# Kernel tuning notes

Measured on AMD Instinct MI355X. Metric: run time of the kernel, lower is better.

Reference implementation:

```python
import jax, jax.numpy as jnp
import numpy as np

B, H, S, D = 4, 16, 2048, 128

def setup_inputs() -> dict:
    key = jax.random.key(0)
    kq, kk, kv = jax.random.split(key, 3)
    query = jax.random.normal(kq, (B, H, S, D), dtype=jnp.float32)
    k = jax.random.normal(kk, (B, H, S, D), dtype=jnp.float32)
    value = jax.random.normal(kv, (B, H, S, D), dtype=jnp.float32)
    attn_mask = jnp.zeros((B, H, S, S), dtype=jnp.float32)
    return {"query": query, "key": k, "value": value, "attn_mask": attn_mask}

def reference(query, key, value, attn_mask):
    # scores: [B,H,S,S]
    scale = 1.0 / jnp.sqrt(jnp.asarray(query.shape[-1], query.dtype))
    scores = jnp.einsum('bhqd,bhkd->bhqk', query, key) * scale + attn_mask
    attn = jax.nn.softmax(scores, axis=-1)
    out = jnp.einsum('bhqk,bhkd->bhqd', attn, value)
    return out
```

## Files before the change

### kernel.cpp

```cpp
#include <hip/hip_runtime.h>

#define SDIM 2048
#define DDIM 128
#define NBH  64
#define BR   128
#define BC   64
#define PSTRIDE 72

using bf16x8 = __attribute__((ext_vector_type(8))) short;
using f32x4  = __attribute__((ext_vector_type(4))) float;

static __device__ __forceinline__ short f2bf(float x) {
    unsigned u = __float_as_uint(x);
    u += 0x7fff + ((u >> 16) & 1);
    return (short)(u >> 16);
}
static __device__ __forceinline__ unsigned pack2(float a, float b) {
    return ((unsigned)(unsigned short)f2bf(a)) |
           (((unsigned)(unsigned short)f2bf(b)) << 16);
}

__global__ __launch_bounds__(256) void kconv_kernel(const float* __restrict__ K,
                                                    unsigned short* __restrict__ Kc)
{
    size_t i = ((size_t)blockIdx.x * 256 + threadIdx.x) * 4;
    float4 v = *(const float4*)(K + i);
    uint2 o;
    o.x = pack2(v.x, v.y);
    o.y = pack2(v.z, v.w);
    *(uint2*)(Kc + i) = o;
}

__global__ __launch_bounds__(256) void vtrans_kernel(const float* __restrict__ V,
                                                     unsigned short* __restrict__ Vt)
{
    __shared__ float t[32][33];
    const int bh = blockIdx.z;
    const int s0 = blockIdx.x * 32;
    const int d0 = blockIdx.y * 32;
    const int x = threadIdx.x & 31;
    const int y = threadIdx.x >> 5;
    const float* Vb = V + (size_t)bh * SDIM * DDIM;
    unsigned short* Vtb = Vt + (size_t)bh * SDIM * DDIM;
#pragma unroll
    for (int i = 0; i < 4; ++i) {
        int r = y + i * 8;
        t[r][x] = Vb[(size_t)(s0 + r) * DDIM + d0 + x];
    }
    __syncthreads();
#pragma unroll
    for (int i = 0; i < 4; ++i) {
        int r = y + i * 8;
        Vtb[(size_t)(d0 + r) * SDIM + s0 + x] = (unsigned short)f2bf(t[x][r]);
    }
}

static __device__ __forceinline__ void load_mask(const float* __restrict__ Mb,
                                                 int q0, int wave, int quad, int n16,
                                                 int kcol, float (&mk)[2][4][4])
{
#pragma unroll
    for (int rt = 0; rt < 2; ++rt) {
        const int rowb = q0 + wave * 32 + rt * 16 + quad * 4;
        const float* mpb = Mb + (size_t)rowb * SDIM + kcol + n16;
#pragma unroll
        for (int ct = 0; ct < 4; ++ct)
#pragma unroll
            for (int r = 0; r < 4; ++r)
                mk[rt][ct][r] = mpb[(size_t)r * SDIM + ct * 16];
    }
}

static __device__ __forceinline__ void ktile_body(
    int k0, int q0, int wave, int quad, int n16, int lane,
    const float* __restrict__ Mb,
    const unsigned short* __restrict__ Kb, const unsigned short* __restrict__ Vb,
    unsigned short* __restrict__ PsW,
    const bf16x8 (&qf)[2][4],
    f32x4 (&acc)[2][8], float (&mrow)[2][4], float (&lrow)[2][4],
    float (&mkc)[2][4][4], float (&mkn)[2][4][4])
{
    const f32x4 zero4 = {0.f, 0.f, 0.f, 0.f};

    f32x4 s[2][4];
#pragma unroll
    for (int rt = 0; rt < 2; ++rt)
#pragma unroll
        for (int ct = 0; ct < 4; ++ct) s[rt][ct] = zero4;
#pragma unroll
    for (int dt = 0; dt < 4; ++dt) {
#pragma unroll
        for (int ct = 0; ct < 4; ++ct) {
            bf16x8 kf = *(const bf16x8*)(Kb + (size_t)(k0 + ct * 16 + n16) * DDIM + dt * 32 + quad * 8);
            s[0][ct] = __builtin_amdgcn_mfma_f32_16x16x32_bf16(qf[0][dt], kf, s[0][ct], 0, 0, 0);
            s[1][ct] = __builtin_amdgcn_mfma_f32_16x16x32_bf16(qf[1][dt], kf, s[1][ct], 0, 0, 0);
        }
    }

    __builtin_amdgcn_sched_barrier(0);
    load_mask(Mb, q0, wave, quad, n16, (k0 + BC) & (SDIM - 1), mkn);
    __builtin_amdgcn_sched_barrier(0);

#pragma unroll
    for (int rt = 0; rt < 2; ++rt)
#pragma unroll
        for (int ct = 0; ct < 4; ++ct)
#pragma unroll
            for (int r = 0; r < 4; ++r)
                s[rt][ct][r] += mkc[rt][ct][r];

    float mx[2][4];
#pragma unroll
    for (int rt = 0; rt < 2; ++rt)
#pragma unroll
        for (int r = 0; r < 4; ++r)
            mx[rt][r] = fmaxf(fmaxf(s[rt][0][r], s[rt][1][r]),
                              fmaxf(s[rt][2][r], s[rt][3][r]));
#pragma unroll
    for (int st = 1; st <= 8; st <<= 1)
#pragma unroll
        for (int rt = 0; rt < 2; ++rt)
#pragma unroll
            for (int r = 0; r < 4; ++r)
                mx[rt][r] = fmaxf(mx[rt][r], __shfl_xor(mx[rt][r], st));

    int anynew = 0;
#pragma unroll
    for (int rt = 0; rt < 2; ++rt)
#pragma unroll
        for (int r = 0; r < 4; ++r)
            anynew |= (mx[rt][r] > mrow[rt][r]) ? 1 : 0;
    if (__ballot(anynew) != 0ull) {
#pragma unroll
        for (int rt = 0; rt < 2; ++rt)
#pragma unroll
            for (int r = 0; r < 4; ++r) {
                float mnew = fmaxf(mrow[rt][r], mx[rt][r]);
                float al = exp2f((mrow[rt][r] - mnew) * 1.44269504f);
                mrow[rt][r] = mnew;
                lrow[rt][r] *= al;
#pragma unroll
                for (int nt = 0; nt < 8; ++nt) acc[rt][nt][r] *= al;
            }
    }

    float rs[2][4];
#pragma unroll
    for (int rt = 0; rt < 2; ++rt)
#pragma unroll
        for (int r = 0; r < 4; ++r) {
            float t = 0.f;
#pragma unroll
            for (int ct = 0; ct < 4; ++ct) {
                float pv = exp2f((s[rt][ct][r] - mrow[rt][r]) * 1.44269504f);
                s[rt][ct][r] = pv;
                t += pv;
            }
            rs[rt][r] = t;
        }
#pragma unroll
    for (int st = 1; st <= 8; st <<= 1)
#pragma unroll
        for (int rt = 0; rt < 2; ++rt)
#pragma unroll
            for (int r = 0; r < 4; ++r)
                rs[rt][r] += __shfl_xor(rs[rt][r], st);
#pragma unroll
    for (int rt = 0; rt < 2; ++rt)
#pragma unroll
        for (int r = 0; r < 4; ++r)
            lrow[rt][r] += rs[rt][r];

#pragma unroll
    for (int rt = 0; rt < 2; ++rt)
#pragma unroll
        for (int ct = 0; ct < 4; ++ct)
#pragma unroll
            for (int r = 0; r < 4; ++r)
                PsW[(rt * 16 + (lane >> 4) * 4 + r) * PSTRIDE + ct * 16 + n16] =
                    (unsigned short)f2bf(s[rt][ct][r]);

    bf16x8 pa[2][2];
#pragma unroll
    for (int rt = 0; rt < 2; ++rt)
#pragma unroll
        for (int kt = 0; kt < 2; ++kt)
            pa[rt][kt] = *(const bf16x8*)(&PsW[(rt * 16 + n16) * PSTRIDE + kt * 32 + quad * 8]);

#pragma unroll
    for (int nt = 0; nt < 8; ++nt) {
#pragma unroll
        for (int kt = 0; kt < 2; ++kt) {
            bf16x8 vf = *(const bf16x8*)(Vb + (size_t)(nt * 16 + n16) * SDIM + k0 + kt * 32 + quad * 8);
            acc[0][nt] = __builtin_amdgcn_mfma_f32_16x16x32_bf16(pa[0][kt], vf, acc[0][nt], 0, 0, 0);
            acc[1][nt] = __builtin_amdgcn_mfma_f32_16x16x32_bf16(pa[1][kt], vf, acc[1][nt], 0, 0, 0);
        }
    }
}

__global__ __launch_bounds__(256, 2) void fattn_kernel(
    const float* __restrict__ Q, const float* __restrict__ M,
    const unsigned short* __restrict__ Kc, const unsigned short* __restrict__ Vt,
    float* __restrict__ O)
{
    const int flat = blockIdx.x;
    const int slot = flat >> 3;
    const int bh   = (flat & 7) * 8 + (slot >> 4);
    const int qt   = slot & 15;

    const int tid  = threadIdx.x;
    const int wave = tid >> 6;
    const int lane = tid & 63;
    const int quad = lane >> 4;
    const int n16  = lane & 15;
    const int q0   = qt * BR;

    const float* Qb = Q + (size_t)bh * SDIM * DDIM;
    const float* Mb = M + (size_t)bh * SDIM * SDIM;
    const unsigned short* Kb = Kc + (size_t)bh * SDIM * DDIM;
    const unsigned short* Vb = Vt + (size_t)bh * SDIM * DDIM;
    float* Ob = O + (size_t)bh * SDIM * DDIM;

    __shared__ __align__(16) unsigned short Ps[4][32 * PSTRIDE];
    unsigned short* PsW = Ps[wave];

    const float scale = 0.08838834764831845f;
    bf16x8 qf[2][4];
#pragma unroll
    for (int rt = 0; rt < 2; ++rt) {
        int row = q0 + wave * 32 + rt * 16 + n16;
        const float* qp = Qb + (size_t)row * DDIM + quad * 8;
#pragma unroll
        for (int dt = 0; dt < 4; ++dt) {
            const float* p = qp + dt * 32;
            float4 a = *(const float4*)p;
            float4 b = *(const float4*)(p + 4);
            bf16x8 f;
            f[0] = f2bf(a.x * scale); f[1] = f2bf(a.y * scale);
            f[2] = f2bf(a.z * scale); f[3] = f2bf(a.w * scale);
            f[4] = f2bf(b.x * scale); f[5] = f2bf(b.y * scale);
            f[6] = f2bf(b.z * scale); f[7] = f2bf(b.w * scale);
            qf[rt][dt] = f;
        }
    }

    f32x4 acc[2][8];
    const f32x4 zero4 = {0.f, 0.f, 0.f, 0.f};
#pragma unroll
    for (int rt = 0; rt < 2; ++rt)
#pragma unroll
        for (int nt = 0; nt < 8; ++nt) acc[rt][nt] = zero4;
    float mrow[2][4], lrow[2][4];
#pragma unroll
    for (int rt = 0; rt < 2; ++rt)
#pragma unroll
        for (int r = 0; r < 4; ++r) { mrow[rt][r] = -1e30f; lrow[rt][r] = 0.f; }

    float mkA[2][4][4], mkB[2][4][4];
    load_mask(Mb, q0, wave, quad, n16, 0, mkA);

#pragma unroll 1
    for (int k0 = 0; k0 < SDIM; k0 += 2 * BC) {
        ktile_body(k0,      q0, wave, quad, n16, lane, Mb, Kb, Vb, PsW,
                   qf, acc, mrow, lrow, mkA, mkB);
        ktile_body(k0 + BC, q0, wave, quad, n16, lane, Mb, Kb, Vb, PsW,
                   qf, acc, mrow, lrow, mkB, mkA);
    }

#pragma unroll
    for (int rt = 0; rt < 2; ++rt) {
#pragma unroll
        for (int r = 0; r < 4; ++r) {
            float inv = 1.0f / lrow[rt][r];
            int row = q0 + wave * 32 + rt * 16 + quad * 4 + r;
            float* op = Ob + (size_t)row * DDIM + n16;
#pragma unroll
            for (int nt = 0; nt < 8; ++nt)
                op[nt * 16] = acc[rt][nt][r] * inv;
        }
    }
}

extern "C" void kernel_launch(void* const* d_in, const int* in_sizes, int n_in,
                              void* d_out, int out_size, void* d_ws, size_t ws_size,
                              hipStream_t stream) {
    const float* Q = (const float*)d_in[0];
    const float* K = (const float*)d_in[1];
    const float* V = (const float*)d_in[2];
    const float* M = (const float*)d_in[3];
    float* O = (float*)d_out;

    unsigned short* Kc = (unsigned short*)d_ws;
    unsigned short* Vt = Kc + (size_t)NBH * SDIM * DDIM;

    size_t nElem = (size_t)NBH * SDIM * DDIM;
    kconv_kernel<<<dim3(nElem / (256 * 4)), 256, 0, stream>>>(K, Kc);
    vtrans_kernel<<<dim3(SDIM / 32, DDIM / 32, NBH), 256, 0, stream>>>(V, Vt);

    fattn_kernel<<<dim3((SDIM / BR) * NBH), 256, 0, stream>>>(Q, M, Kc, Vt, O);
}
```

Before: 1.983 ms.

## Scan attention mask once and skip per-tile mask loads when all zero

Adds a grid-stride kernel that ORs the bits of the whole mask into a workspace flag, which the K-conversion kernel resets first. The attention kernel reads the flag and runs a template variant with no mask loads or adds when the mask is all zero. It keeps the masked variant as a fallback and also preloads all K fragments per tile into registers before the MFMAs. The mask is still read in full once, but as a plain bandwidth-bound stream rather than strided loads inside the attention loop. The price is an extra launch, more register pressure, and dropping the previous one-tile-ahead mask prefetch in the masked path.

```diff
diff --git a/kernel.cpp b/kernel.cpp
--- a/kernel.cpp
+++ b/kernel.cpp
@@ -21,8 +21,10 @@
 }
 
 __global__ __launch_bounds__(256) void kconv_kernel(const float* __restrict__ K,
-                                                    unsigned short* __restrict__ Kc)
-{
+                                                    unsigned short* __restrict__ Kc,
+                                                    unsigned* __restrict__ flag)
+{
+    if (flag != nullptr && blockIdx.x == 0 && threadIdx.x == 0) *flag = 0u;
     size_t i = ((size_t)blockIdx.x * 256 + threadIdx.x) * 4;
     float4 v = *(const float4*)(K + i);
     uint2 o;
@@ -55,6 +57,19 @@
     }
 }
 
+__global__ __launch_bounds__(256) void maskscan_kernel(const uint4* __restrict__ M4,
+                                                       unsigned* __restrict__ flag)
+{
+    const size_t n4 = (size_t)NBH * SDIM * SDIM / 4;
+    unsigned acc = 0;
+    for (size_t i = (size_t)blockIdx.x * 256 + threadIdx.x; i < n4;
+         i += (size_t)gridDim.x * 256) {
+        uint4 v = M4[i];
+        acc |= v.x | v.y | v.z | v.w;
+    }
+    if (acc) *flag = 1u;
+}
+
 static __device__ __forceinline__ void load_mask(const float* __restrict__ Mb,
                                                  int q0, int wave, int quad, int n16,
                                                  int kcol, float (&mk)[2][4][4])
@@ -71,17 +86,28 @@
     }
 }
 
+template<bool MASKED>
 static __device__ __forceinline__ void ktile_body(
     int k0, int q0, int wave, int quad, int n16, int lane,
     const float* __restrict__ Mb,
     const unsigned short* __restrict__ Kb, const unsigned short* __restrict__ Vb,
     unsigned short* __restrict__ PsW,
     const bf16x8 (&qf)[2][4],
-    f32x4 (&acc)[2][8], float (&mrow)[2][4], float (&lrow)[2][4],
-    float (&mkc)[2][4][4], float (&mkn)[2][4][4])
+    f32x4 (&acc)[2][8], float (&mrow)[2][4], float (&lrow)[2][4])
 {
     const f32x4 zero4 = {0.f, 0.f, 0.f, 0.f};
 
+    bf16x8 kfr[4][4];
+#pragma unroll
+    for (int dt = 0; dt < 4; ++dt)
+#pragma unroll
+        for (int ct = 0; ct < 4; ++ct)
+            kfr[dt][ct] = *(const bf16x8*)(Kb + (size_t)(k0 + ct * 16 + n16) * DDIM + dt * 32 + quad * 8);
+
+    float mk[2][4][4];
+    if constexpr (MASKED)
+        load_mask(Mb, q0, wave, quad, n16, k0, mk);
+
     f32x4 s[2][4];
 #pragma unroll
     for (int rt = 0; rt < 2; ++rt)
@@ -91,23 +117,20 @@
     for (int dt = 0; dt < 4; ++dt) {
 #pragma unroll
         for (int ct = 0; ct < 4; ++ct) {
-            bf16x8 kf = *(const bf16x8*)(Kb + (size_t)(k0 + ct * 16 + n16) * DDIM + dt * 32 + quad * 8);
-            s[0][ct] = __builtin_amdgcn_mfma_f32_16x16x32_bf16(qf[0][dt], kf, s[0][ct], 0, 0, 0);
-            s[1][ct] = __builtin_amdgcn_mfma_f32_16x16x32_bf16(qf[1][dt], kf, s[1][ct], 0, 0, 0);
-        }
-    }
-
-    __builtin_amdgcn_sched_barrier(0);
-    load_mask(Mb, q0, wave, quad, n16, (k0 + BC) & (SDIM - 1), mkn);
-    __builtin_amdgcn_sched_barrier(0);
-
-#pragma unroll
-    for (int rt = 0; rt < 2; ++rt)
-#pragma unroll
-        for (int ct = 0; ct < 4; ++ct)
-#pragma unroll
-            for (int r = 0; r < 4; ++r)
-                s[rt][ct][r] += mkc[rt][ct][r];
+            s[0][ct] = __builtin_amdgcn_mfma_f32_16x16x32_bf16(qf[0][dt], kfr[dt][ct], s[0][ct], 0, 0, 0);
+            s[1][ct] = __builtin_amdgcn_mfma_f32_16x16x32_bf16(qf[1][dt], kfr[dt][ct], s[1][ct], 0, 0, 0);
+        }
+    }
+
+    if constexpr (MASKED) {
+#pragma unroll
+        for (int rt = 0; rt < 2; ++rt)
+#pragma unroll
+            for (int ct = 0; ct < 4; ++ct)
+#pragma unroll
+                for (int r = 0; r < 4; ++r)
+                    s[rt][ct][r] += mk[rt][ct][r];
+    }
 
     float mx[2][4];
 #pragma unroll
@@ -201,6 +224,7 @@
 __global__ __launch_bounds__(256, 2) void fattn_kernel(
     const float* __restrict__ Q, const float* __restrict__ M,
     const unsigned short* __restrict__ Kc, const unsigned short* __restrict__ Vt,
+    const unsigned* __restrict__ flag,
     float* __restrict__ O)
 {
     const int flat = blockIdx.x;
@@ -220,6 +244,8 @@
     const unsigned short* Kb = Kc + (size_t)bh * SDIM * DDIM;
     const unsigned short* Vb = Vt + (size_t)bh * SDIM * DDIM;
     float* Ob = O + (size_t)bh * SDIM * DDIM;
+
+    const bool masked = (flag == nullptr) || (*flag != 0u);
 
     __shared__ __align__(16) unsigned short Ps[4][32 * PSTRIDE];
     unsigned short* PsW = Ps[wave];
@@ -256,15 +282,16 @@
 #pragma unroll
         for (int r = 0; r < 4; ++r) { mrow[rt][r] = -1e30f; lrow[rt][r] = 0.f; }
 
-    float mkA[2][4][4], mkB[2][4][4];
-    load_mask(Mb, q0, wave, quad, n16, 0, mkA);
-
+    if (!masked) {
 #pragma unroll 1
-    for (int k0 = 0; k0 < SDIM; k0 += 2 * BC) {
-        ktile_body(k0,      q0, wave, quad, n16, lane, Mb, Kb, Vb, PsW,
-                   qf, acc, mrow, lrow, mkA, mkB);
-        ktile_body(k0 + BC, q0, wave, quad, n16, lane, Mb, Kb, Vb, PsW,
-                   qf, acc, mrow, lrow, mkB, mkA);
+        for (int k0 = 0; k0 < SDIM; k0 += BC)
+            ktile_body<false>(k0, q0, wave, quad, n16, lane, Mb, Kb, Vb, PsW,
+                              qf, acc, mrow, lrow);
+    } else {
+#pragma unroll 1
+        for (int k0 = 0; k0 < SDIM; k0 += BC)
+            ktile_body<true>(k0, q0, wave, quad, n16, lane, Mb, Kb, Vb, PsW,
+                             qf, acc, mrow, lrow);
     }
 
 #pragma unroll
@@ -290,12 +317,18 @@
     const float* M = (const float*)d_in[3];
     float* O = (float*)d_out;
 
+    const size_t nElem = (size_t)NBH * SDIM * DDIM;
     unsigned short* Kc = (unsigned short*)d_ws;
-    unsigned short* Vt = Kc + (size_t)NBH * SDIM * DDIM;
-
-    size_t nElem = (size_t)NBH * SDIM * DDIM;
-    kconv_kernel<<<dim3(nElem / (256 * 4)), 256, 0, stream>>>(K, Kc);
+    unsigned short* Vt = Kc + nElem;
+
+    const size_t kvBytes = 2 * nElem * sizeof(unsigned short);
+    unsigned* flag = (ws_size >= kvBytes + sizeof(unsigned))
+                   ? (unsigned*)((char*)d_ws + kvBytes) : nullptr;
+
+    kconv_kernel<<<dim3(nElem / (256 * 4)), 256, 0, stream>>>(K, Kc, flag);
     vtrans_kernel<<<dim3(SDIM / 32, DDIM / 32, NBH), 256, 0, stream>>>(V, Vt);
-
-    fattn_kernel<<<dim3((SDIM / BR) * NBH), 256, 0, stream>>>(Q, M, Kc, Vt, O);
-}
+    if (flag != nullptr)
+        maskscan_kernel<<<dim3(2048), 256, 0, stream>>>((const uint4*)M, flag);
+
+    fattn_kernel<<<dim3((SDIM / BR) * NBH), 256, 0, stream>>>(Q, M, Kc, Vt, flag, O);
+}
```

Measured after the change: 1.938 ms. 2.3% less time.
